# Performance work log

Hardware: AMD Instinct MI355X
Metric: run time of the kernel (lower is better)

The kernel has to match this reference:

```python
import math
import jax, jax.numpy as jnp
import numpy as np

N_NODES = 100000
N_EDGES = 1600000
IN_DIM = 512
HID = 128
OUT_DIM = 1
N_LAYERS = 8
ALPHA = 0.1
THETA = 0.5


def setup_inputs() -> dict:
    key = jax.random.key(0)
    ks = jax.random.split(key, 8)
    x = jax.random.normal(ks[0], (N_NODES, IN_DIM), dtype=jnp.float32)
    edge_index = jax.random.randint(ks[1], (2, N_EDGES), 0, N_NODES, dtype=jnp.int64)
    edge_weight = jax.random.uniform(ks[2], (N_EDGES,), dtype=jnp.float32)
    s_in = 1.0 / math.sqrt(IN_DIM)
    s_h = 1.0 / math.sqrt(HID)
    W_in = jax.random.uniform(ks[3], (IN_DIM, HID), jnp.float32, -s_in, s_in)
    b_in = jax.random.uniform(ks[4], (HID,), jnp.float32, -s_in, s_in)
    W_layers = jax.random.uniform(ks[5], (N_LAYERS, HID, HID), jnp.float32, -s_h, s_h)
    W_out = jax.random.uniform(ks[6], (HID, OUT_DIM), jnp.float32, -s_h, s_h)
    b_out = jax.random.uniform(ks[7], (OUT_DIM,), jnp.float32, -s_h, s_h)
    return {"x": x, "edge_index": edge_index, "edge_weight": edge_weight,
            "W_in": W_in, "b_in": b_in, "W_layers": W_layers,
            "W_out": W_out, "b_out": b_out}


def _gcn_norm(edge_index, n_nodes, dtype):
    # gcn_norm with add_self_loops=True and unit edge weights
    # (GCN2Net never forwards edge_weight into GCN2Conv).
    loop = jnp.arange(n_nodes, dtype=edge_index.dtype)
    src = jnp.concatenate([edge_index[0], loop])
    dst = jnp.concatenate([edge_index[1], loop])
    w = jnp.ones(src.shape[0], dtype=dtype)
    deg = jax.ops.segment_sum(w, dst, num_segments=n_nodes)
    dinv = jnp.where(deg > 0, jax.lax.rsqrt(deg), 0.0).astype(dtype)
    norm = dinv[src] * w * dinv[dst]
    return src, dst, norm


def reference(x, edge_index, edge_weight, W_in, b_in, W_layers, W_out, b_out):
    n = x.shape[0]
    src, dst, norm = _gcn_norm(edge_index, n, x.dtype)

    x = x @ W_in + b_in          # initial_proj: [N, HID]
    x0 = x
    for i in range(N_LAYERS):
        # sparse neighbor aggregation: A_hat @ x
        agg = jax.ops.segment_sum(x[src] * norm[:, None], dst, num_segments=n)
        # initial residual
        h = (1.0 - ALPHA) * agg + ALPHA * x0
        # identity mapping (shared_weights=True): (1-beta)*h + beta*(h @ W)
        beta = math.log(THETA / (i + 1) + 1.0)
        x = (1.0 - beta) * h + beta * (h @ W_layers[i])
        x = jax.nn.relu(x)
        # dropout omitted (eval mode / drop_prob=0)
    return x @ W_out + b_out     # final_proj: [N, OUT_DIM]
```

## Files before the change

kernel.cpp:

```cpp
#include <hip/hip_runtime.h>
#include <math.h>

#define NN 100000
#define NE 1600000
#define IN_DIM 512
#define HID 128
#define N_LAYERS 8
#define NB 98
#define PADMAX 3200000

typedef __attribute__((ext_vector_type(4))) float f32x4;
typedef __attribute__((ext_vector_type(8))) _Float16 h16x8;
typedef __attribute__((ext_vector_type(2))) _Float16 h16x2;


__global__ void deg_count_kernel(const int* __restrict__ dst, int* __restrict__ deg) {
    int e = blockIdx.x * blockDim.x + threadIdx.x;
    if (e < NE) atomicAdd(&deg[dst[e]], 1);
}

__global__ void dinv_kernel(const int* __restrict__ deg, float* __restrict__ dinv) {
    int i = blockIdx.x * blockDim.x + threadIdx.x;
    if (i < NN) dinv[i] = rsqrtf((float)(deg[i] + 1));
}

__global__ void scan1_kernel(const int* __restrict__ deg, int* __restrict__ bsum) {
    __shared__ int s[16];
    int gi = blockIdx.x * 1024 + threadIdx.x;
    int d = (gi < NN) ? deg[gi] : 0;
    int r = (d + 15) & ~15;
    for (int off = 32; off; off >>= 1) r += __shfl_down(r, off, 64);
    if ((threadIdx.x & 63) == 0) s[threadIdx.x >> 6] = r;
    __syncthreads();
    if (threadIdx.x == 0) {
        int t = 0;
        for (int i = 0; i < 16; ++i) t += s[i];
        bsum[blockIdx.x] = t;
    }
}

__global__ void scan2_kernel(const int* __restrict__ bsum, int* __restrict__ boff,
                             int* __restrict__ row_ptr) {
    __shared__ int s[128];
    int tid = threadIdx.x;
    int v = (tid < NB) ? bsum[tid] : 0;
    s[tid] = v;
    __syncthreads();
    for (int off = 1; off < 128; off <<= 1) {
        int t = (tid >= off) ? s[tid - off] : 0;
        __syncthreads();
        s[tid] += t;
        __syncthreads();
    }
    if (tid < NB) boff[tid] = s[tid] - v;
    if (tid == NB - 1) row_ptr[NN] = s[tid];
}

__global__ void scan3_kernel(const int* __restrict__ deg, const int* __restrict__ boff,
                             int* __restrict__ row_ptr, int* __restrict__ cursor) {
    __shared__ int s[1024];
    int tid = threadIdx.x;
    int gi = blockIdx.x * 1024 + tid;
    int d = (gi < NN) ? deg[gi] : 0;
    int v = (d + 15) & ~15;
    s[tid] = v;
    __syncthreads();
    for (int off = 1; off < 1024; off <<= 1) {
        int t = (tid >= off) ? s[tid - off] : 0;
        __syncthreads();
        s[tid] += t;
        __syncthreads();
    }
    if (gi < NN) {
        int o = boff[blockIdx.x] + s[tid] - v;
        row_ptr[gi] = o;
        cursor[gi]  = o;
    }
}

__global__ void pad_kernel(const int* __restrict__ deg, const int* __restrict__ row_ptr,
                           int* __restrict__ col, float* __restrict__ val) {
    int i = blockIdx.x * 256 + threadIdx.x;
    if (i < NN) {
        int d = deg[i];
        int s = row_ptr[i] + d;
        int e = row_ptr[i] + ((d + 15) & ~15);
        for (int p = s; p < e; ++p) { col[p] = 0; val[p] = 0.f; }
    }
}

__global__ void fill_kernel(const int* __restrict__ src, const int* __restrict__ dst,
                            const float* __restrict__ dinv, int* __restrict__ cursor,
                            int* __restrict__ col, float* __restrict__ val) {
    int e = blockIdx.x * blockDim.x + threadIdx.x;
    if (e < NE) {
        int s = src[e], d = dst[e];
        int pos = atomicAdd(&cursor[d], 1);
        col[pos] = s;
        val[pos] = dinv[s] * dinv[d];
    }
}


__global__ void wprep_init_kernel(const float* __restrict__ W,
                                  _Float16* __restrict__ Bhi, _Float16* __restrict__ Blo) {
    int t = blockIdx.x * 256 + threadIdx.x;
    if (t >= 8 * 16 * 64) return;
    int lane = t & 63, nkk = t >> 6;
    int n = nkk >> 4, kk = nkk & 15;
    int scol = n * 16 + (lane & 15);
    int sr0 = kk * 32 + (lane >> 4) * 8;
#pragma unroll
    for (int j = 0; j < 8; ++j) {
        float w = W[(size_t)(sr0 + j) * HID + scol];
        _Float16 hi = (_Float16)w;
        _Float16 lo = (_Float16)(w - (float)hi);
        Bhi[(size_t)t * 8 + j] = hi;
        Blo[(size_t)t * 8 + j] = lo;
    }
}

__global__ void wprep_layers_kernel(const float* __restrict__ WL,
                                    _Float16* __restrict__ Bhi, _Float16* __restrict__ Blo) {
    int t = blockIdx.x * 256 + threadIdx.x;
    if (t >= N_LAYERS * 8 * 4 * 64) return;
    int layer = t >> 11;
    int r = t & 2047;
    int lane = r & 63, nkk = r >> 6;
    int n = nkk >> 2, kk = nkk & 3;
    const float* W = WL + (size_t)layer * HID * HID;
    int scol = n * 16 + (lane & 15);
    int sr0 = kk * 32 + (lane >> 4) * 8;
#pragma unroll
    for (int j = 0; j < 8; ++j) {
        float w = W[(size_t)(sr0 + j) * HID + scol];
        _Float16 hi = (_Float16)w;
        _Float16 lo = (_Float16)(w - (float)hi);
        Bhi[(size_t)t * 8 + j] = hi;
        Blo[(size_t)t * 8 + j] = lo;
    }
}


__device__ inline int xsw(int row, int blk) {
    return row * 512 + ((blk ^ (row & 7)) << 3);
}

__global__ __launch_bounds__(512) void init_mfma_kernel(
    const float* __restrict__ x, const h16x8* __restrict__ Bhi, const h16x8* __restrict__ Blo,
    const float* __restrict__ b, _Float16* __restrict__ cur, _Float16* __restrict__ x0h) {
    __shared__ _Float16 xs[64 * 512];
    int t = threadIdx.x;
    int row0 = blockIdx.x * 64;

#pragma unroll
    for (int i = 0; i < 8; ++i) {
        int c = t + 512 * i;
        int row = c >> 6, blk = c & 63;
        int grow = row0 + row; if (grow >= NN) grow = NN - 1;
        const float* p = x + (size_t)grow * IN_DIM + blk * 8;
        float4 v0 = *(const float4*)p;
        float4 v1 = *(const float4*)(p + 4);
        h16x8 h;
        h[0] = (_Float16)v0.x; h[1] = (_Float16)v0.y;
        h[2] = (_Float16)v0.z; h[3] = (_Float16)v0.w;
        h[4] = (_Float16)v1.x; h[5] = (_Float16)v1.y;
        h[6] = (_Float16)v1.z; h[7] = (_Float16)v1.w;
        *(h16x8*)&xs[xsw(row, blk)] = h;
    }
    __syncthreads();

    int lane = t & 63, wid = t >> 6;
    int rsel = lane & 15, ksel = lane >> 4;

    f32x4 acc[4];
#pragma unroll
    for (int m = 0; m < 4; ++m) acc[m] = (f32x4){0.f, 0.f, 0.f, 0.f};

#pragma unroll
    for (int kk = 0; kk < 16; ++kk) {
        h16x8 bh = Bhi[(wid * 16 + kk) * 64 + lane];
        h16x8 bl = Blo[(wid * 16 + kk) * 64 + lane];
#pragma unroll
        for (int m = 0; m < 4; ++m) {
            h16x8 a = *(const h16x8*)&xs[xsw(m * 16 + rsel, kk * 4 + ksel)];
            acc[m] = __builtin_amdgcn_mfma_f32_16x16x32_f16(a, bh, acc[m], 0, 0, 0);
            acc[m] = __builtin_amdgcn_mfma_f32_16x16x32_f16(a, bl, acc[m], 0, 0, 0);
        }
    }

    int col = wid * 16 + rsel;
    float bias = b[col];
#pragma unroll
    for (int m = 0; m < 4; ++m) {
#pragma unroll
        for (int r = 0; r < 4; ++r) {
            int row = row0 + m * 16 + ksel * 4 + r;
            if (row < NN) {
                float v = acc[m][r] + bias;
                _Float16 hv = (_Float16)v;
                cur[(size_t)row * HID + col] = hv;
                x0h[(size_t)row * HID + col] = hv;
            }
        }
    }
}


__device__ inline int hsw(int row, int blk) {
    return row * 128 + ((blk ^ (row & 7)) << 3);
}

__global__ __launch_bounds__(512) void fused_layer_kernel(
    const _Float16* __restrict__ x, const _Float16* __restrict__ x0,
    const int* __restrict__ row_ptr, const int* __restrict__ col,
    const float* __restrict__ val, const float* __restrict__ dinv,
    const h16x8* __restrict__ Bhi, const h16x8* __restrict__ Blo,
    float beta, _Float16* __restrict__ out) {
    __shared__ _Float16 hs[64 * 128];
    int t = threadIdx.x;
    int lane = t & 63, wid = t >> 6;
    int node0 = blockIdx.x * 64;

    h16x8 bh[4], bl[4];
#pragma unroll
    for (int kk = 0; kk < 4; ++kk) {
        bh[kk] = Bhi[(wid * 4 + kk) * 64 + lane];
        bl[kk] = Blo[(wid * 4 + kk) * 64 + lane];
    }

    int g = lane >> 4, q = lane & 15;
    const h16x8* x8 = (const h16x8*)x;
    for (int i = 0; i < 8; ++i) {
        int lrow = wid * 8 + i;
        int node = node0 + lrow;
        if (node < NN) {
            float di = dinv[node];
            h16x8 sv = x8[(size_t)node * 16 + q];
            h16x8 zv = ((const h16x8*)x0)[(size_t)node * 16 + q];
            float acc[8];
#pragma unroll
            for (int j = 0; j < 8; ++j) acc[j] = 0.f;
            int p1 = row_ptr[node + 1];
            for (int p = row_ptr[node]; p < p1; p += 16) {
                int4   c4 = *(const int4*)(col + p + 4 * g);
                float4 w4 = *(const float4*)(val + p + 4 * g);
                h16x8 v0 = x8[(size_t)c4.x * 16 + q];
                h16x8 v1 = x8[(size_t)c4.y * 16 + q];
                h16x8 v2 = x8[(size_t)c4.z * 16 + q];
                h16x8 v3 = x8[(size_t)c4.w * 16 + q];
#pragma unroll
                for (int j = 0; j < 8; ++j)
                    acc[j] += w4.x * (float)v0[j] + w4.y * (float)v1[j]
                            + w4.z * (float)v2[j] + w4.w * (float)v3[j];
            }
#pragma unroll
            for (int j = 0; j < 8; ++j) {
                acc[j] += __shfl_xor(acc[j], 16, 64);
                acc[j] += __shfl_xor(acc[j], 32, 64);
            }
            if (g == 0) {
                float d2 = di * di;
                h16x8 o16;
#pragma unroll
                for (int j = 0; j < 8; ++j)
                    o16[j] = (_Float16)(0.9f * (acc[j] + d2 * (float)sv[j]) + 0.1f * (float)zv[j]);
                *(h16x8*)&hs[hsw(lrow, q)] = o16;
            }
        } else if (g == 0) {
            h16x8 z;
#pragma unroll
            for (int j = 0; j < 8; ++j) z[j] = (_Float16)0.f;
            *(h16x8*)&hs[hsw(lrow, q)] = z;
        }
    }
    __syncthreads();

    int rsel = lane & 15, ksel = lane >> 4;
    f32x4 acc[4];
#pragma unroll
    for (int m = 0; m < 4; ++m) acc[m] = (f32x4){0.f, 0.f, 0.f, 0.f};

#pragma unroll
    for (int m = 0; m < 4; ++m)
#pragma unroll
        for (int kk = 0; kk < 4; ++kk) {
            h16x8 a = *(const h16x8*)&hs[hsw(m * 16 + rsel, kk * 4 + ksel)];
            acc[m] = __builtin_amdgcn_mfma_f32_16x16x32_f16(a, bh[kk], acc[m], 0, 0, 0);
            acc[m] = __builtin_amdgcn_mfma_f32_16x16x32_f16(a, bl[kk], acc[m], 0, 0, 0);
        }

    float ob = 1.0f - beta;
    int colw = wid * 16 + rsel;
#pragma unroll
    for (int m = 0; m < 4; ++m) {
#pragma unroll
        for (int r = 0; r < 4; ++r) {
            int lr = m * 16 + ksel * 4 + r;
            int row = node0 + lr;
            if (row < NN) {
                float h = (float)hs[lr * 128 + (((colw >> 3) ^ (lr & 7)) << 3) + (colw & 7)];
                float v = ob * h + beta * acc[m][r];
                v = v > 0.f ? v : 0.f;
                out[(size_t)row * HID + colw] = (_Float16)v;
            }
        }
    }
}


__global__ __launch_bounds__(256) void final16_kernel(
    const _Float16* __restrict__ x, const float* __restrict__ Wout,
    const float* __restrict__ bout, float* __restrict__ out) {
    int node = blockIdx.x * 4 + (threadIdx.x >> 6);
    int lane = threadIdx.x & 63;
    h16x2 a = ((const h16x2*)x)[(size_t)node * 64 + lane];
    float2 w = ((const float2*)Wout)[lane];
    float v = (float)a[0] * w.x + (float)a[1] * w.y;
#pragma unroll
    for (int off = 32; off; off >>= 1) v += __shfl_down(v, off, 64);
    if (lane == 0) out[node] = v + bout[0];
}


extern "C" void kernel_launch(void* const* d_in, const int* in_sizes, int n_in,
                              void* d_out, int out_size, void* d_ws, size_t ws_size,
                              hipStream_t stream) {
    const float* x_in     = (const float*)d_in[0];
    const int*   ei       = (const int*)d_in[1];
    const float* W_in     = (const float*)d_in[3];
    const float* b_in     = (const float*)d_in[4];
    const float* W_layers = (const float*)d_in[5];
    const float* W_out    = (const float*)d_in[6];
    const float* b_out    = (const float*)d_in[7];
    float* out = (float*)d_out;

    const int* src = ei;
    const int* dst = ei + NE;

    char* ws = (char*)d_ws;
    size_t off = 0;
    auto alloc = [&](size_t bytes) {
        size_t p = off;
        off = (off + bytes + 255) & ~(size_t)255;
        return p;
    };
    int*   deg     = (int*)(ws + alloc((size_t)NN * 4));
    float* dinv    = (float*)(ws + alloc((size_t)NN * 4));
    int*   row_ptr = (int*)(ws + alloc((size_t)(NN + 1) * 4));
    int*   cursor  = (int*)(ws + alloc((size_t)NN * 4));
    int*   bsum    = (int*)(ws + alloc((size_t)NB * 4));
    int*   boff    = (int*)(ws + alloc((size_t)NB * 4));
    int*   col     = (int*)(ws + alloc((size_t)PADMAX * 4));
    float* val     = (float*)(ws + alloc((size_t)PADMAX * 4));
    _Float16* x0h  = (_Float16*)(ws + alloc((size_t)NN * HID * 2));
    _Float16* bufA = (_Float16*)(ws + alloc((size_t)NN * HID * 2));
    _Float16* bufB = (_Float16*)(ws + alloc((size_t)NN * HID * 2));
    _Float16* Bhi0 = (_Float16*)(ws + alloc((size_t)IN_DIM * HID * 2));
    _Float16* Blo0 = (_Float16*)(ws + alloc((size_t)IN_DIM * HID * 2));
    _Float16* BhiL = (_Float16*)(ws + alloc((size_t)N_LAYERS * HID * HID * 2));
    _Float16* BloL = (_Float16*)(ws + alloc((size_t)N_LAYERS * HID * HID * 2));

    hipMemsetAsync(deg, 0, (size_t)NN * 4, stream);

    deg_count_kernel<<<NE / 256, 256, 0, stream>>>(dst, deg);
    dinv_kernel<<<(NN + 255) / 256, 256, 0, stream>>>(deg, dinv);
    scan1_kernel<<<NB, 1024, 0, stream>>>(deg, bsum);
    scan2_kernel<<<1, 128, 0, stream>>>(bsum, boff, row_ptr);
    scan3_kernel<<<NB, 1024, 0, stream>>>(deg, boff, row_ptr, cursor);
    pad_kernel<<<(NN + 255) / 256, 256, 0, stream>>>(deg, row_ptr, col, val);
    fill_kernel<<<NE / 256, 256, 0, stream>>>(src, dst, dinv, cursor, col, val);

    wprep_init_kernel<<<32, 256, 0, stream>>>(W_in, Bhi0, Blo0);
    wprep_layers_kernel<<<64, 256, 0, stream>>>(W_layers, BhiL, BloL);

    init_mfma_kernel<<<(NN + 63) / 64, 512, 0, stream>>>(
        x_in, (const h16x8*)Bhi0, (const h16x8*)Blo0, b_in, bufA, x0h);

    _Float16* cur = bufA;
    _Float16* nxt = bufB;
    for (int l = 0; l < N_LAYERS; ++l) {
        float beta = logf(0.5f / (float)(l + 1) + 1.0f);
        fused_layer_kernel<<<(NN + 63) / 64, 512, 0, stream>>>(
            cur, x0h, row_ptr, col, val, dinv,
            (const h16x8*)(BhiL + (size_t)l * HID * HID),
            (const h16x8*)(BloL + (size_t)l * HID * HID), beta, nxt);
        _Float16* tmp = cur; cur = nxt; nxt = tmp;
    }

    final16_kernel<<<NN / 4, 256, 0, stream>>>(cur, W_out, b_out, out);
}
```

Measured before the change: 1.037 ms.

## Fold symmetric normalization into pre-scaled features, drop per-edge weight array

```diff
diff --git a/kernel.cpp b/kernel.cpp
--- a/kernel.cpp
+++ b/kernel.cpp
@@ -79,26 +79,30 @@
 }
 
 __global__ void pad_kernel(const int* __restrict__ deg, const int* __restrict__ row_ptr,
-                           int* __restrict__ col, float* __restrict__ val) {
+                           int* __restrict__ col) {
     int i = blockIdx.x * 256 + threadIdx.x;
     if (i < NN) {
         int d = deg[i];
         int s = row_ptr[i] + d;
         int e = row_ptr[i] + ((d + 15) & ~15);
-        for (int p = s; p < e; ++p) { col[p] = 0; val[p] = 0.f; }
+        for (int p = s; p < e; ++p) col[p] = NN;
     }
 }
 
 __global__ void fill_kernel(const int* __restrict__ src, const int* __restrict__ dst,
-                            const float* __restrict__ dinv, int* __restrict__ cursor,
-                            int* __restrict__ col, float* __restrict__ val) {
+                            int* __restrict__ cursor, int* __restrict__ col) {
     int e = blockIdx.x * blockDim.x + threadIdx.x;
     if (e < NE) {
         int s = src[e], d = dst[e];
         int pos = atomicAdd(&cursor[d], 1);
         col[pos] = s;
-        val[pos] = dinv[s] * dinv[d];
-    }
+    }
+}
+
+__global__ void zero_sentinel_kernel(_Float16* __restrict__ a, _Float16* __restrict__ b) {
+    int t = threadIdx.x;
+    a[(size_t)NN * HID + t] = (_Float16)0.f;
+    b[(size_t)NN * HID + t] = (_Float16)0.f;
 }
 
 
@@ -148,7 +152,8 @@
 
 __global__ __launch_bounds__(512) void init_mfma_kernel(
     const float* __restrict__ x, const h16x8* __restrict__ Bhi, const h16x8* __restrict__ Blo,
-    const float* __restrict__ b, _Float16* __restrict__ cur, _Float16* __restrict__ x0h) {
+    const float* __restrict__ b, const float* __restrict__ dinv,
+    _Float16* __restrict__ ycur, _Float16* __restrict__ x0h) {
     __shared__ _Float16 xs[64 * 512];
     int t = threadIdx.x;
     int row0 = blockIdx.x * 64;
@@ -198,9 +203,9 @@
             int row = row0 + m * 16 + ksel * 4 + r;
             if (row < NN) {
                 float v = acc[m][r] + bias;
-                _Float16 hv = (_Float16)v;
-                cur[(size_t)row * HID + col] = hv;
-                x0h[(size_t)row * HID + col] = hv;
+                float di = dinv[row];
+                ycur[(size_t)row * HID + col] = (_Float16)(di * v);
+                x0h[(size_t)row * HID + col]  = (_Float16)v;
             }
         }
     }
@@ -212,11 +217,11 @@
 }
 
 __global__ __launch_bounds__(512) void fused_layer_kernel(
-    const _Float16* __restrict__ x, const _Float16* __restrict__ x0,
+    const _Float16* __restrict__ y, const _Float16* __restrict__ x0,
     const int* __restrict__ row_ptr, const int* __restrict__ col,
-    const float* __restrict__ val, const float* __restrict__ dinv,
+    const float* __restrict__ dinv,
     const h16x8* __restrict__ Bhi, const h16x8* __restrict__ Blo,
-    float beta, _Float16* __restrict__ out) {
+    float beta, _Float16* __restrict__ yout) {
     __shared__ _Float16 hs[64 * 128];
     int t = threadIdx.x;
     int lane = t & 63, wid = t >> 6;
@@ -230,7 +235,7 @@
     }
 
     int g = lane >> 4, q = lane & 15;
-    const h16x8* x8 = (const h16x8*)x;
+    const h16x8* x8 = (const h16x8*)y;
     for (int i = 0; i < 8; ++i) {
         int lrow = wid * 8 + i;
         int node = node0 + lrow;
@@ -243,16 +248,14 @@
             for (int j = 0; j < 8; ++j) acc[j] = 0.f;
             int p1 = row_ptr[node + 1];
             for (int p = row_ptr[node]; p < p1; p += 16) {
-                int4   c4 = *(const int4*)(col + p + 4 * g);
-                float4 w4 = *(const float4*)(val + p + 4 * g);
+                int4 c4 = *(const int4*)(col + p + 4 * g);
                 h16x8 v0 = x8[(size_t)c4.x * 16 + q];
                 h16x8 v1 = x8[(size_t)c4.y * 16 + q];
                 h16x8 v2 = x8[(size_t)c4.z * 16 + q];
                 h16x8 v3 = x8[(size_t)c4.w * 16 + q];
 #pragma unroll
                 for (int j = 0; j < 8; ++j)
-                    acc[j] += w4.x * (float)v0[j] + w4.y * (float)v1[j]
-                            + w4.z * (float)v2[j] + w4.w * (float)v3[j];
+                    acc[j] += (float)v0[j] + (float)v1[j] + (float)v2[j] + (float)v3[j];
             }
 #pragma unroll
             for (int j = 0; j < 8; ++j) {
@@ -260,11 +263,12 @@
                 acc[j] += __shfl_xor(acc[j], 32, 64);
             }
             if (g == 0) {
-                float d2 = di * di;
                 h16x8 o16;
 #pragma unroll
-                for (int j = 0; j < 8; ++j)
-                    o16[j] = (_Float16)(0.9f * (acc[j] + d2 * (float)sv[j]) + 0.1f * (float)zv[j]);
+                for (int j = 0; j < 8; ++j) {
+                    float s = acc[j] + (float)sv[j];
+                    o16[j] = (_Float16)(0.9f * (di * s) + 0.1f * (float)zv[j]);
+                }
                 *(h16x8*)&hs[hsw(lrow, q)] = o16;
             }
         } else if (g == 0) {
@@ -302,7 +306,7 @@
                 float h = (float)hs[lr * 128 + (((colw >> 3) ^ (lr & 7)) << 3) + (colw & 7)];
                 float v = ob * h + beta * acc[m][r];
                 v = v > 0.f ? v : 0.f;
-                out[(size_t)row * HID + colw] = (_Float16)v;
+                yout[(size_t)row * HID + colw] = (_Float16)(dinv[row] * v);
             }
         }
     }
@@ -310,16 +314,17 @@
 
 
 __global__ __launch_bounds__(256) void final16_kernel(
-    const _Float16* __restrict__ x, const float* __restrict__ Wout,
-    const float* __restrict__ bout, float* __restrict__ out) {
+    const _Float16* __restrict__ y, const int* __restrict__ deg,
+    const float* __restrict__ Wout, const float* __restrict__ bout,
+    float* __restrict__ out) {
     int node = blockIdx.x * 4 + (threadIdx.x >> 6);
     int lane = threadIdx.x & 63;
-    h16x2 a = ((const h16x2*)x)[(size_t)node * 64 + lane];
+    h16x2 a = ((const h16x2*)y)[(size_t)node * 64 + lane];
     float2 w = ((const float2*)Wout)[lane];
     float v = (float)a[0] * w.x + (float)a[1] * w.y;
 #pragma unroll
     for (int off = 32; off; off >>= 1) v += __shfl_down(v, off, 64);
-    if (lane == 0) out[node] = v + bout[0];
+    if (lane == 0) out[node] = v * sqrtf((float)(deg[node] + 1)) + bout[0];
 }
 
 
@@ -352,10 +357,9 @@
     int*   bsum    = (int*)(ws + alloc((size_t)NB * 4));
     int*   boff    = (int*)(ws + alloc((size_t)NB * 4));
     int*   col     = (int*)(ws + alloc((size_t)PADMAX * 4));
-    float* val     = (float*)(ws + alloc((size_t)PADMAX * 4));
     _Float16* x0h  = (_Float16*)(ws + alloc((size_t)NN * HID * 2));
-    _Float16* bufA = (_Float16*)(ws + alloc((size_t)NN * HID * 2));
-    _Float16* bufB = (_Float16*)(ws + alloc((size_t)NN * HID * 2));
+    _Float16* bufA = (_Float16*)(ws + alloc((size_t)(NN + 16) * HID * 2));
+    _Float16* bufB = (_Float16*)(ws + alloc((size_t)(NN + 16) * HID * 2));
     _Float16* Bhi0 = (_Float16*)(ws + alloc((size_t)IN_DIM * HID * 2));
     _Float16* Blo0 = (_Float16*)(ws + alloc((size_t)IN_DIM * HID * 2));
     _Float16* BhiL = (_Float16*)(ws + alloc((size_t)N_LAYERS * HID * HID * 2));
@@ -368,25 +372,26 @@
     scan1_kernel<<<NB, 1024, 0, stream>>>(deg, bsum);
     scan2_kernel<<<1, 128, 0, stream>>>(bsum, boff, row_ptr);
     scan3_kernel<<<NB, 1024, 0, stream>>>(deg, boff, row_ptr, cursor);
-    pad_kernel<<<(NN + 255) / 256, 256, 0, stream>>>(deg, row_ptr, col, val);
-    fill_kernel<<<NE / 256, 256, 0, stream>>>(src, dst, dinv, cursor, col, val);
+    pad_kernel<<<(NN + 255) / 256, 256, 0, stream>>>(deg, row_ptr, col);
+    fill_kernel<<<NE / 256, 256, 0, stream>>>(src, dst, cursor, col);
+    zero_sentinel_kernel<<<1, 128, 0, stream>>>(bufA, bufB);
 
     wprep_init_kernel<<<32, 256, 0, stream>>>(W_in, Bhi0, Blo0);
     wprep_layers_kernel<<<64, 256, 0, stream>>>(W_layers, BhiL, BloL);
 
     init_mfma_kernel<<<(NN + 63) / 64, 512, 0, stream>>>(
-        x_in, (const h16x8*)Bhi0, (const h16x8*)Blo0, b_in, bufA, x0h);
+        x_in, (const h16x8*)Bhi0, (const h16x8*)Blo0, b_in, dinv, bufA, x0h);
 
     _Float16* cur = bufA;
     _Float16* nxt = bufB;
     for (int l = 0; l < N_LAYERS; ++l) {
         float beta = logf(0.5f / (float)(l + 1) + 1.0f);
         fused_layer_kernel<<<(NN + 63) / 64, 512, 0, stream>>>(
-            cur, x0h, row_ptr, col, val, dinv,
+            cur, x0h, row_ptr, col, dinv,
             (const h16x8*)(BhiL + (size_t)l * HID * HID),
             (const h16x8*)(BloL + (size_t)l * HID * HID), beta, nxt);
         _Float16* tmp = cur; cur = nxt; nxt = tmp;
     }
 
-    final16_kernel<<<NN / 4, 256, 0, stream>>>(cur, W_out, b_out, out);
-}
+    final16_kernel<<<NN / 4, 256, 0, stream>>>(cur, deg, W_out, b_out, out);
+}
```

After: 1.058 ms. 2.0% more time.
